# Kernel tuning notes

Hardware: AMD Instinct MI355X
Metric: run time of the kernel (lower is better)

Reference implementation:

```python
import jax, jax.numpy as jnp
import numpy as np

H = 768  # sparse grid height
W = 768  # sparse grid width
N = 200000  # active sites
CIN = 256
CB = 64


def setup_inputs() -> dict:
    key = jax.random.key(0)
    ks = jax.random.split(key, 11)
    rng = np.random.default_rng(0)
    # unique active-site linear coordinates on the HxW grid
    coords = jnp.asarray(np.sort(rng.choice(H * W, N, replace=False)).astype(np.int64))
    feats = jax.random.normal(ks[0], (N, CIN), jnp.float32)
    w1 = jax.random.normal(ks[1], (CIN, CB), jnp.float32) / np.float32(np.sqrt(CIN))
    w2 = jax.random.normal(ks[2], (9, CB, CB), jnp.float32) / np.float32(np.sqrt(9 * CB))
    w3 = jax.random.normal(ks[3], (CB, CIN), jnp.float32) / np.float32(np.sqrt(CB))
    s1 = jax.random.uniform(ks[4], (CB,), jnp.float32, 0.5, 1.5)
    b1 = jax.random.normal(ks[5], (CB,), jnp.float32) * 0.1
    s2 = jax.random.uniform(ks[6], (CB,), jnp.float32, 0.5, 1.5)
    b2 = jax.random.normal(ks[7], (CB,), jnp.float32) * 0.1
    s3 = jax.random.uniform(ks[8], (CIN,), jnp.float32, 0.5, 1.5)
    b3 = jax.random.normal(ks[9], (CIN,), jnp.float32) * 0.1
    return dict(feats=feats, coords=coords, w1=w1, w2=w2, w3=w3,
                s1=s1, b1=b1, s2=s2, b2=b2, s3=s3, b3=b3)


def sparse_conv3x3(feats, coords, w2):
    # active-site sparse 3x3 conv: gather valid neighbors, matmul per tap, accumulate
    idx_map = jnp.full((H * W,), -1, jnp.int32).at[coords].set(
        jnp.arange(N, dtype=jnp.int32))
    y, x = coords // W, coords % W
    out = jnp.zeros((N, w2.shape[2]), feats.dtype)
    k = 0
    for dy in (-1, 0, 1):
        for dx in (-1, 0, 1):
            ny, nx = y + dy, x + dx
            inb = (ny >= 0) & (ny < H) & (nx >= 0) & (nx < W)
            lin = jnp.clip(ny, 0, H - 1) * W + jnp.clip(nx, 0, W - 1)
            r = idx_map[lin]
            ok = inb & (r >= 0)
            g = jnp.where(ok[:, None], feats[jnp.maximum(r, 0)], 0.0)
            out = out + g @ w2[k]
            k += 1
    return out


def reference(feats, coords, w1, w2, w3, s1, b1, s2, b2, s3, b3):
    identity = feats
    out = jax.nn.relu((feats @ w1) * s1 + b1)            # conv1 1x1 + bn1 + relu
    out = jax.nn.relu(sparse_conv3x3(out, coords, w2) * s2 + b2)  # conv2 3x3 + bn2 + relu
    out = (out @ w3) * s3 + b3                            # conv3 1x1 + bn3
    return jax.nn.relu(out + identity)                    # residual + relu
```

## Files before the change

kernel.cpp:

```cpp
#include <hip/hip_runtime.h>
#include <hip/hip_bf16.h>
#include <stdint.h>

#define HH 768
#define WW 768
#define NN 200000
#define CI 256
#define CB 64

typedef __attribute__((ext_vector_type(8))) __bf16 bf16x8;
typedef __attribute__((ext_vector_type(4))) float f32x4;

__device__ inline unsigned short f2bf(float f) {
    union { float f; unsigned int i; } v; v.f = f;
    unsigned int r = v.i + 0x7FFF + ((v.i >> 16) & 1);
    return (unsigned short)(r >> 16);
}
__device__ inline f32x4 mfma16(bf16x8 a, bf16x8 b, f32x4 c) {
    return __builtin_amdgcn_mfma_f32_16x16x32_bf16(a, b, c, 0, 0, 0);
}
__device__ inline bf16x8 ldfrag(const unsigned short* p) {
    return *(const bf16x8*)p;
}
__device__ inline bf16x8 ldfrag_f32(const float* p) {
    float4 f0 = *(const float4*)(p);
    float4 f1 = *(const float4*)(p + 4);
    bf16x8 a;
    a[0] = (__bf16)f0.x; a[1] = (__bf16)f0.y; a[2] = (__bf16)f0.z; a[3] = (__bf16)f0.w;
    a[4] = (__bf16)f1.x; a[5] = (__bf16)f1.y; a[6] = (__bf16)f1.z; a[7] = (__bf16)f1.w;
    return a;
}


__global__ void k_scatter(const int* __restrict__ coords, int* __restrict__ idx_map) {
    int i = blockIdx.x * 256 + threadIdx.x;
    if (i < NN) idx_map[coords[i]] = i;
}

__global__ void k_prepw(const float* __restrict__ w1,
                        const float* __restrict__ w2,
                        const float* __restrict__ w3,
                        unsigned short* __restrict__ w1t,
                        unsigned short* __restrict__ w2t,
                        unsigned short* __restrict__ w3t) {
    int tid = blockIdx.x * 256 + threadIdx.x;
    int stride = gridDim.x * 256;
    for (int i = tid; i < CI * CB; i += stride) {
        int k = i / CB, n = i % CB;
        w1t[n * CI + k] = f2bf(w1[i]);
    }
    for (int i = tid; i < 9 * CB * CB; i += stride) {
        int t = i / (CB * CB), rem = i % (CB * CB);
        int k = rem / CB, n = rem % CB;
        w2t[t * CB * CB + n * CB + k] = f2bf(w2[i]);
    }
    for (int i = tid; i < CB * CI; i += stride) {
        int k = i / CI, n = i % CI;
        w3t[n * CB + k] = f2bf(w3[i]);
    }
}


__global__ __launch_bounds__(256, 2) void k_gemm1(const float* __restrict__ feats,
                                                  const unsigned short* __restrict__ w1t,
                                                  const float* __restrict__ s1,
                                                  const float* __restrict__ b1,
                                                  unsigned short* __restrict__ out1) {
    const int wave = threadIdx.x >> 6;
    const int lane = threadIdx.x & 63;
    const int m = lane & 15;
    const int quad = lane >> 4;
    const int gw = blockIdx.x * 4 + wave;
    if (gw >= NN / 64) return;
    const int row0 = gw * 64;

    f32x4 acc[4][4];
#pragma unroll
    for (int mt = 0; mt < 4; ++mt)
#pragma unroll
        for (int nt = 0; nt < 4; ++nt) acc[mt][nt] = (f32x4){0.f, 0.f, 0.f, 0.f};

#pragma unroll
    for (int ks = 0; ks < 8; ++ks) {
        bf16x8 a[4];
#pragma unroll
        for (int mt = 0; mt < 4; ++mt)
            a[mt] = ldfrag_f32(feats + (size_t)(row0 + mt * 16 + m) * CI + quad * 8 + ks * 32);
#pragma unroll
        for (int nt = 0; nt < 4; ++nt) {
            bf16x8 b = ldfrag(w1t + (nt * 16 + m) * CI + quad * 8 + ks * 32);
#pragma unroll
            for (int mt = 0; mt < 4; ++mt)
                acc[mt][nt] = mfma16(a[mt], b, acc[mt][nt]);
        }
    }

#pragma unroll
    for (int mt = 0; mt < 4; ++mt)
#pragma unroll
        for (int nt = 0; nt < 4; ++nt) {
            int col = nt * 16 + m;
            float sc = s1[col], bi = b1[col];
#pragma unroll
            for (int r = 0; r < 4; ++r) {
                int orow = row0 + mt * 16 + quad * 4 + r;
                float v = acc[mt][nt][r] * sc + bi;
                v = v > 0.f ? v : 0.f;
                out1[orow * CB + col] = f2bf(v);
            }
        }
}


__global__ __launch_bounds__(256, 2) void k_conv(const unsigned short* __restrict__ out1,
                                                 const unsigned short* __restrict__ w2t,
                                                 const int* __restrict__ coords,
                                                 const int* __restrict__ idx_map,
                                                 const float* __restrict__ s2,
                                                 const float* __restrict__ b2,
                                                 const unsigned short* __restrict__ zrow,
                                                 unsigned short* __restrict__ out2) {
    __shared__ int s_nbr[256 * 9];
    const int tid = threadIdx.x;
    const int grow = blockIdx.x * 256 + tid;
    if (grow < NN) {
        int c = coords[grow];
        int y = c / WW, x = c - y * WW;
#pragma unroll
        for (int t = 0; t < 9; ++t) {
            int dy = t / 3 - 1, dx = t % 3 - 1;
            int ny = y + dy, nx = x + dx;
            int r = -1;
            if (ny >= 0 && ny < HH && nx >= 0 && nx < WW) r = idx_map[ny * WW + nx];
            s_nbr[tid * 9 + t] = r;
        }
    } else {
#pragma unroll
        for (int t = 0; t < 9; ++t) s_nbr[tid * 9 + t] = -1;
    }
    __syncthreads();

    const int wave = tid >> 6;
    const int lane = tid & 63;
    const int m = lane & 15;
    const int quad = lane >> 4;
    const int row0 = blockIdx.x * 256 + wave * 64;
    if (row0 >= NN) return;

    f32x4 acc[4][4];
#pragma unroll
    for (int mt = 0; mt < 4; ++mt)
#pragma unroll
        for (int nt = 0; nt < 4; ++nt) acc[mt][nt] = (f32x4){0.f, 0.f, 0.f, 0.f};

#pragma unroll
    for (int t = 0; t < 9; ++t) {
        bf16x8 a[4][2];
#pragma unroll
        for (int mt = 0; mt < 4; ++mt) {
            int r = s_nbr[(wave * 64 + mt * 16 + m) * 9 + t];
            const unsigned short* base = (r >= 0) ? (out1 + (size_t)r * CB) : zrow;
            a[mt][0] = ldfrag(base + quad * 8);
            a[mt][1] = ldfrag(base + quad * 8 + 32);
        }
#pragma unroll
        for (int ks = 0; ks < 2; ++ks)
#pragma unroll
            for (int nt = 0; nt < 4; ++nt) {
                bf16x8 b = ldfrag(w2t + t * CB * CB + (nt * 16 + m) * CB + quad * 8 + ks * 32);
#pragma unroll
                for (int mt = 0; mt < 4; ++mt)
                    acc[mt][nt] = mfma16(a[mt][ks], b, acc[mt][nt]);
            }
    }

#pragma unroll
    for (int mt = 0; mt < 4; ++mt)
#pragma unroll
        for (int nt = 0; nt < 4; ++nt) {
            int col = nt * 16 + m;
            float sc = s2[col], bi = b2[col];
#pragma unroll
            for (int r = 0; r < 4; ++r) {
                int orow = row0 + mt * 16 + quad * 4 + r;
                float v = acc[mt][nt][r] * sc + bi;
                v = v > 0.f ? v : 0.f;
                out2[orow * CB + col] = f2bf(v);
            }
        }
}


__global__ __launch_bounds__(256, 2) void k_gemm3(const unsigned short* __restrict__ out2,
                                                  const unsigned short* __restrict__ w3t,
                                                  const float* __restrict__ s3,
                                                  const float* __restrict__ b3,
                                                  const float* __restrict__ feats,
                                                  float* __restrict__ out) {
    const int wave = threadIdx.x >> 6;
    const int lane = threadIdx.x & 63;
    const int m = lane & 15;
    const int quad = lane >> 4;
    const int row0 = blockIdx.x * 64;
    const int col0 = wave * 64;

    f32x4 acc[4][4];
#pragma unroll
    for (int mt = 0; mt < 4; ++mt)
#pragma unroll
        for (int nt = 0; nt < 4; ++nt) acc[mt][nt] = (f32x4){0.f, 0.f, 0.f, 0.f};

    bf16x8 a[4][2];
#pragma unroll
    for (int mt = 0; mt < 4; ++mt) {
        const unsigned short* ap = out2 + (size_t)(row0 + mt * 16 + m) * CB + quad * 8;
        a[mt][0] = ldfrag(ap);
        a[mt][1] = ldfrag(ap + 32);
    }
#pragma unroll
    for (int ks = 0; ks < 2; ++ks)
#pragma unroll
        for (int nt = 0; nt < 4; ++nt) {
            bf16x8 b = ldfrag(w3t + (col0 + nt * 16 + m) * CB + quad * 8 + ks * 32);
#pragma unroll
            for (int mt = 0; mt < 4; ++mt)
                acc[mt][nt] = mfma16(a[mt][ks], b, acc[mt][nt]);
        }

#pragma unroll
    for (int mt = 0; mt < 4; ++mt)
#pragma unroll
        for (int nt = 0; nt < 4; ++nt) {
            int col = col0 + nt * 16 + m;
            float sc = s3[col], bi = b3[col];
#pragma unroll
            for (int r = 0; r < 4; ++r) {
                int orow = row0 + mt * 16 + quad * 4 + r;
                float v = acc[mt][nt][r] * sc + bi + feats[(size_t)orow * CI + col];
                v = v > 0.f ? v : 0.f;
                out[(size_t)orow * CI + col] = v;
            }
        }
}


extern "C" void kernel_launch(void* const* d_in, const int* in_sizes, int n_in,
                              void* d_out, int out_size, void* d_ws, size_t ws_size,
                              hipStream_t stream) {
    const float* feats = (const float*)d_in[0];
    const int* coords = (const int*)d_in[1];
    const float* w1 = (const float*)d_in[2];
    const float* w2 = (const float*)d_in[3];
    const float* w3 = (const float*)d_in[4];
    const float* s1 = (const float*)d_in[5];
    const float* b1 = (const float*)d_in[6];
    const float* s2 = (const float*)d_in[7];
    const float* b2 = (const float*)d_in[8];
    const float* s3 = (const float*)d_in[9];
    const float* b3 = (const float*)d_in[10];
    float* out = (float*)d_out;

    char* ws = (char*)d_ws;
    int* idx_map        = (int*)(ws + 0);
    unsigned short* w1t = (unsigned short*)(ws + 2359296);
    unsigned short* w2t = (unsigned short*)(ws + 2392064);
    unsigned short* w3t = (unsigned short*)(ws + 2465792);
    unsigned short* out1= (unsigned short*)(ws + 2498560);
    unsigned short* out2= (unsigned short*)(ws + 28098560);
    unsigned short* zrow= (unsigned short*)(ws + 53698560);

    hipMemsetAsync(idx_map, 0xFF, (size_t)HH * WW * 4, stream);
    hipMemsetAsync(zrow, 0x00, 128, stream);
    k_scatter<<<(NN + 255) / 256, 256, 0, stream>>>(coords, idx_map);
    k_prepw<<<64, 256, 0, stream>>>(w1, w2, w3, w1t, w2t, w3t);
    k_gemm1<<<(NN / 64 + 3) / 4, 256, 0, stream>>>(feats, w1t, s1, b1, out1);
    k_conv<<<(NN + 255) / 256, 256, 0, stream>>>(out1, w2t, coords, idx_map, s2, b2, zrow, out2);
    k_gemm3<<<NN / 64, 256, 0, stream>>>(out2, w3t, s3, b3, feats, out);
}
```

Before: 521.3 us.

## Swap MFMA operands for vectorized epilogue stores and shrink per-wave row tiles

Swaps the A/B operands of the MFMA so each lane holds 4 consecutive output columns of one row. The epilogues can then write 4-element vector stores (bf16x4, float4) and read scale, bias and residual as float4, instead of scattered scalar stores. Each wave's row tile drops from 64 to 32 rows with launch_bounds raised to 4 waves per SIMD, which cuts register pressure and increases occupancy and grid size. gemm3 now loops over four column chunks per wave instead of splitting columns across waves. The trade-off is less reuse of each weight fragment per load and more total weight reads.

```diff
diff --git a/kernel.cpp b/kernel.cpp
--- a/kernel.cpp
+++ b/kernel.cpp
@@ -10,6 +10,7 @@
 
 typedef __attribute__((ext_vector_type(8))) __bf16 bf16x8;
 typedef __attribute__((ext_vector_type(4))) float f32x4;
+typedef __attribute__((ext_vector_type(4))) unsigned short u16x4;
 
 __device__ inline unsigned short f2bf(float f) {
     union { float f; unsigned int i; } v; v.f = f;
@@ -61,7 +62,7 @@
 }
 
 
-__global__ __launch_bounds__(256, 2) void k_gemm1(const float* __restrict__ feats,
+__global__ __launch_bounds__(256, 4) void k_gemm1(const float* __restrict__ feats,
                                                   const unsigned short* __restrict__ w1t,
                                                   const float* __restrict__ s1,
                                                   const float* __restrict__ b1,
@@ -70,49 +71,53 @@
     const int lane = threadIdx.x & 63;
     const int m = lane & 15;
     const int quad = lane >> 4;
-    const int gw = blockIdx.x * 4 + wave;
-    if (gw >= NN / 64) return;
-    const int row0 = gw * 64;
-
-    f32x4 acc[4][4];
-#pragma unroll
-    for (int mt = 0; mt < 4; ++mt)
-#pragma unroll
-        for (int nt = 0; nt < 4; ++nt) acc[mt][nt] = (f32x4){0.f, 0.f, 0.f, 0.f};
+    const int row0 = blockIdx.x * 128 + wave * 32;
+    if (row0 >= NN) return;
+
+    f32x4 acc[2][4];
+#pragma unroll
+    for (int rt = 0; rt < 2; ++rt)
+#pragma unroll
+        for (int ct = 0; ct < 4; ++ct) acc[rt][ct] = (f32x4){0.f, 0.f, 0.f, 0.f};
 
 #pragma unroll
     for (int ks = 0; ks < 8; ++ks) {
-        bf16x8 a[4];
-#pragma unroll
-        for (int mt = 0; mt < 4; ++mt)
-            a[mt] = ldfrag_f32(feats + (size_t)(row0 + mt * 16 + m) * CI + quad * 8 + ks * 32);
-#pragma unroll
-        for (int nt = 0; nt < 4; ++nt) {
-            bf16x8 b = ldfrag(w1t + (nt * 16 + m) * CI + quad * 8 + ks * 32);
-#pragma unroll
-            for (int mt = 0; mt < 4; ++mt)
-                acc[mt][nt] = mfma16(a[mt], b, acc[mt][nt]);
-        }
-    }
-
-#pragma unroll
-    for (int mt = 0; mt < 4; ++mt)
-#pragma unroll
-        for (int nt = 0; nt < 4; ++nt) {
-            int col = nt * 16 + m;
-            float sc = s1[col], bi = b1[col];
-#pragma unroll
-            for (int r = 0; r < 4; ++r) {
-                int orow = row0 + mt * 16 + quad * 4 + r;
-                float v = acc[mt][nt][r] * sc + bi;
-                v = v > 0.f ? v : 0.f;
-                out1[orow * CB + col] = f2bf(v);
-            }
-        }
-}
-
-
-__global__ __launch_bounds__(256, 2) void k_conv(const unsigned short* __restrict__ out1,
+        bf16x8 f[2];
+#pragma unroll
+        for (int rt = 0; rt < 2; ++rt)
+            f[rt] = ldfrag_f32(feats + (size_t)(row0 + rt * 16 + m) * CI + quad * 8 + ks * 32);
+#pragma unroll
+        for (int ct = 0; ct < 4; ++ct) {
+            bf16x8 b = ldfrag(w1t + (ct * 16 + m) * CI + quad * 8 + ks * 32);
+#pragma unroll
+            for (int rt = 0; rt < 2; ++rt)
+                acc[rt][ct] = mfma16(b, f[rt], acc[rt][ct]);
+        }
+    }
+
+#pragma unroll
+    for (int rt = 0; rt < 2; ++rt)
+#pragma unroll
+        for (int ct = 0; ct < 4; ++ct) {
+            int row = row0 + rt * 16 + m;
+            int c0 = ct * 16 + quad * 4;
+            float4 sc = *(const float4*)(s1 + c0);
+            float4 bi = *(const float4*)(b1 + c0);
+            float v0 = acc[rt][ct][0] * sc.x + bi.x;
+            float v1 = acc[rt][ct][1] * sc.y + bi.y;
+            float v2 = acc[rt][ct][2] * sc.z + bi.z;
+            float v3 = acc[rt][ct][3] * sc.w + bi.w;
+            u16x4 o;
+            o.x = f2bf(v0 > 0.f ? v0 : 0.f);
+            o.y = f2bf(v1 > 0.f ? v1 : 0.f);
+            o.z = f2bf(v2 > 0.f ? v2 : 0.f);
+            o.w = f2bf(v3 > 0.f ? v3 : 0.f);
+            *(u16x4*)(out1 + (size_t)row * CB + c0) = o;
+        }
+}
+
+
+__global__ __launch_bounds__(256, 4) void k_conv(const unsigned short* __restrict__ out1,
                                                  const unsigned short* __restrict__ w2t,
                                                  const int* __restrict__ coords,
                                                  const int* __restrict__ idx_map,
@@ -120,23 +125,25 @@
                                                  const float* __restrict__ b2,
                                                  const unsigned short* __restrict__ zrow,
                                                  unsigned short* __restrict__ out2) {
-    __shared__ int s_nbr[256 * 9];
+    __shared__ int s_nbr[128 * 9];
     const int tid = threadIdx.x;
-    const int grow = blockIdx.x * 256 + tid;
-    if (grow < NN) {
-        int c = coords[grow];
-        int y = c / WW, x = c - y * WW;
-#pragma unroll
-        for (int t = 0; t < 9; ++t) {
-            int dy = t / 3 - 1, dx = t % 3 - 1;
-            int ny = y + dy, nx = x + dx;
-            int r = -1;
-            if (ny >= 0 && ny < HH && nx >= 0 && nx < WW) r = idx_map[ny * WW + nx];
-            s_nbr[tid * 9 + t] = r;
-        }
-    } else {
-#pragma unroll
-        for (int t = 0; t < 9; ++t) s_nbr[tid * 9 + t] = -1;
+    if (tid < 128) {
+        int grow = blockIdx.x * 128 + tid;
+        if (grow < NN) {
+            int c = coords[grow];
+            int y = c / WW, x = c - y * WW;
+#pragma unroll
+            for (int t = 0; t < 9; ++t) {
+                int dy = t / 3 - 1, dx = t % 3 - 1;
+                int ny = y + dy, nx = x + dx;
+                int r = -1;
+                if (ny >= 0 && ny < HH && nx >= 0 && nx < WW) r = idx_map[ny * WW + nx];
+                s_nbr[tid * 9 + t] = r;
+            }
+        } else {
+#pragma unroll
+            for (int t = 0; t < 9; ++t) s_nbr[tid * 9 + t] = -1;
+        }
     }
     __syncthreads();
 
@@ -144,54 +151,59 @@
     const int lane = tid & 63;
     const int m = lane & 15;
     const int quad = lane >> 4;
-    const int row0 = blockIdx.x * 256 + wave * 64;
+    const int row0 = blockIdx.x * 128 + wave * 32;
     if (row0 >= NN) return;
 
-    f32x4 acc[4][4];
-#pragma unroll
-    for (int mt = 0; mt < 4; ++mt)
-#pragma unroll
-        for (int nt = 0; nt < 4; ++nt) acc[mt][nt] = (f32x4){0.f, 0.f, 0.f, 0.f};
+    f32x4 acc[2][4];
+#pragma unroll
+    for (int rt = 0; rt < 2; ++rt)
+#pragma unroll
+        for (int ct = 0; ct < 4; ++ct) acc[rt][ct] = (f32x4){0.f, 0.f, 0.f, 0.f};
 
 #pragma unroll
     for (int t = 0; t < 9; ++t) {
-        bf16x8 a[4][2];
-#pragma unroll
-        for (int mt = 0; mt < 4; ++mt) {
-            int r = s_nbr[(wave * 64 + mt * 16 + m) * 9 + t];
+        bf16x8 a[2][2];
+#pragma unroll
+        for (int rt = 0; rt < 2; ++rt) {
+            int r = s_nbr[(wave * 32 + rt * 16 + m) * 9 + t];
             const unsigned short* base = (r >= 0) ? (out1 + (size_t)r * CB) : zrow;
-            a[mt][0] = ldfrag(base + quad * 8);
-            a[mt][1] = ldfrag(base + quad * 8 + 32);
+            a[rt][0] = ldfrag(base + quad * 8);
+            a[rt][1] = ldfrag(base + quad * 8 + 32);
         }
 #pragma unroll
         for (int ks = 0; ks < 2; ++ks)
 #pragma unroll
-            for (int nt = 0; nt < 4; ++nt) {
-                bf16x8 b = ldfrag(w2t + t * CB * CB + (nt * 16 + m) * CB + quad * 8 + ks * 32);
-#pragma unroll
-                for (int mt = 0; mt < 4; ++mt)
-                    acc[mt][nt] = mfma16(a[mt][ks], b, acc[mt][nt]);
+            for (int ct = 0; ct < 4; ++ct) {
+                bf16x8 b = ldfrag(w2t + t * CB * CB + (ct * 16 + m) * CB + quad * 8 + ks * 32);
+#pragma unroll
+                for (int rt = 0; rt < 2; ++rt)
+                    acc[rt][ct] = mfma16(b, a[rt][ks], acc[rt][ct]);
             }
     }
 
 #pragma unroll
-    for (int mt = 0; mt < 4; ++mt)
-#pragma unroll
-        for (int nt = 0; nt < 4; ++nt) {
-            int col = nt * 16 + m;
-            float sc = s2[col], bi = b2[col];
-#pragma unroll
-            for (int r = 0; r < 4; ++r) {
-                int orow = row0 + mt * 16 + quad * 4 + r;
-                float v = acc[mt][nt][r] * sc + bi;
-                v = v > 0.f ? v : 0.f;
-                out2[orow * CB + col] = f2bf(v);
-            }
-        }
-}
-
-
-__global__ __launch_bounds__(256, 2) void k_gemm3(const unsigned short* __restrict__ out2,
+    for (int rt = 0; rt < 2; ++rt)
+#pragma unroll
+        for (int ct = 0; ct < 4; ++ct) {
+            int row = row0 + rt * 16 + m;
+            int c0 = ct * 16 + quad * 4;
+            float4 sc = *(const float4*)(s2 + c0);
+            float4 bi = *(const float4*)(b2 + c0);
+            float v0 = acc[rt][ct][0] * sc.x + bi.x;
+            float v1 = acc[rt][ct][1] * sc.y + bi.y;
+            float v2 = acc[rt][ct][2] * sc.z + bi.z;
+            float v3 = acc[rt][ct][3] * sc.w + bi.w;
+            u16x4 o;
+            o.x = f2bf(v0 > 0.f ? v0 : 0.f);
+            o.y = f2bf(v1 > 0.f ? v1 : 0.f);
+            o.z = f2bf(v2 > 0.f ? v2 : 0.f);
+            o.w = f2bf(v3 > 0.f ? v3 : 0.f);
+            *(u16x4*)(out2 + (size_t)row * CB + c0) = o;
+        }
+}
+
+
+__global__ __launch_bounds__(256, 4) void k_gemm3(const unsigned short* __restrict__ out2,
                                                   const unsigned short* __restrict__ w3t,
                                                   const float* __restrict__ s3,
                                                   const float* __restrict__ b3,
@@ -201,46 +213,57 @@
     const int lane = threadIdx.x & 63;
     const int m = lane & 15;
     const int quad = lane >> 4;
-    const int row0 = blockIdx.x * 64;
-    const int col0 = wave * 64;
-
-    f32x4 acc[4][4];
-#pragma unroll
-    for (int mt = 0; mt < 4; ++mt)
-#pragma unroll
-        for (int nt = 0; nt < 4; ++nt) acc[mt][nt] = (f32x4){0.f, 0.f, 0.f, 0.f};
-
-    bf16x8 a[4][2];
-#pragma unroll
-    for (int mt = 0; mt < 4; ++mt) {
-        const unsigned short* ap = out2 + (size_t)(row0 + mt * 16 + m) * CB + quad * 8;
-        a[mt][0] = ldfrag(ap);
-        a[mt][1] = ldfrag(ap + 32);
-    }
-#pragma unroll
-    for (int ks = 0; ks < 2; ++ks)
-#pragma unroll
-        for (int nt = 0; nt < 4; ++nt) {
-            bf16x8 b = ldfrag(w3t + (col0 + nt * 16 + m) * CB + quad * 8 + ks * 32);
-#pragma unroll
-            for (int mt = 0; mt < 4; ++mt)
-                acc[mt][nt] = mfma16(a[mt][ks], b, acc[mt][nt]);
-        }
-
-#pragma unroll
-    for (int mt = 0; mt < 4; ++mt)
-#pragma unroll
-        for (int nt = 0; nt < 4; ++nt) {
-            int col = col0 + nt * 16 + m;
-            float sc = s3[col], bi = b3[col];
-#pragma unroll
-            for (int r = 0; r < 4; ++r) {
-                int orow = row0 + mt * 16 + quad * 4 + r;
-                float v = acc[mt][nt][r] * sc + bi + feats[(size_t)orow * CI + col];
-                v = v > 0.f ? v : 0.f;
-                out[(size_t)orow * CI + col] = v;
+    const int row0 = blockIdx.x * 128 + wave * 32;
+    if (row0 >= NN) return;
+
+    bf16x8 arow[2][2];
+#pragma unroll
+    for (int rt = 0; rt < 2; ++rt) {
+        const unsigned short* ap = out2 + (size_t)(row0 + rt * 16 + m) * CB + quad * 8;
+        arow[rt][0] = ldfrag(ap);
+        arow[rt][1] = ldfrag(ap + 32);
+    }
+
+#pragma unroll
+    for (int cc = 0; cc < 4; ++cc) {
+        const int cbase = cc * 64;
+        f32x4 acc[2][4];
+#pragma unroll
+        for (int rt = 0; rt < 2; ++rt)
+#pragma unroll
+            for (int ct = 0; ct < 4; ++ct) acc[rt][ct] = (f32x4){0.f, 0.f, 0.f, 0.f};
+
+#pragma unroll
+        for (int ks = 0; ks < 2; ++ks)
+#pragma unroll
+            for (int ct = 0; ct < 4; ++ct) {
+                bf16x8 b = ldfrag(w3t + (cbase + ct * 16 + m) * CB + quad * 8 + ks * 32);
+#pragma unroll
+                for (int rt = 0; rt < 2; ++rt)
+                    acc[rt][ct] = mfma16(b, arow[rt][ks], acc[rt][ct]);
             }
-        }
+
+#pragma unroll
+        for (int rt = 0; rt < 2; ++rt)
+#pragma unroll
+            for (int ct = 0; ct < 4; ++ct) {
+                int row = row0 + rt * 16 + m;
+                int c0 = cbase + ct * 16 + quad * 4;
+                float4 sc = *(const float4*)(s3 + c0);
+                float4 bi = *(const float4*)(b3 + c0);
+                float4 fr = *(const float4*)(feats + (size_t)row * CI + c0);
+                float4 v;
+                v.x = acc[rt][ct][0] * sc.x + bi.x + fr.x;
+                v.y = acc[rt][ct][1] * sc.y + bi.y + fr.y;
+                v.z = acc[rt][ct][2] * sc.z + bi.z + fr.z;
+                v.w = acc[rt][ct][3] * sc.w + bi.w + fr.w;
+                v.x = v.x > 0.f ? v.x : 0.f;
+                v.y = v.y > 0.f ? v.y : 0.f;
+                v.z = v.z > 0.f ? v.z : 0.f;
+                v.w = v.w > 0.f ? v.w : 0.f;
+                *(float4*)(out + (size_t)row * CI + c0) = v;
+            }
+    }
 }
 
 
@@ -273,7 +296,7 @@
     hipMemsetAsync(zrow, 0x00, 128, stream);
     k_scatter<<<(NN + 255) / 256, 256, 0, stream>>>(coords, idx_map);
     k_prepw<<<64, 256, 0, stream>>>(w1, w2, w3, w1t, w2t, w3t);
-    k_gemm1<<<(NN / 64 + 3) / 4, 256, 0, stream>>>(feats, w1t, s1, b1, out1);
-    k_conv<<<(NN + 255) / 256, 256, 0, stream>>>(out1, w2t, coords, idx_map, s2, b2, zrow, out2);
-    k_gemm3<<<NN / 64, 256, 0, stream>>>(out2, w3t, s3, b3, feats, out);
-}
+    k_gemm1<<<(NN + 127) / 128, 256, 0, stream>>>(feats, w1t, s1, b1, out1);
+    k_conv<<<(NN + 127) / 128, 256, 0, stream>>>(out1, w2t, coords, idx_map, s2, b2, zrow, out2);
+    k_gemm3<<<(NN + 127) / 128, 256, 0, stream>>>(out2, w3t, s3, b3, feats, out);
+}
```

Measured after the change: 582.1 us. 11.7% more time.
